# Kernel optimization log

Measured on AMD Instinct MI355X. Metric: run time of the kernel, lower is better.

Reference implementation:

```python
import jax, jax.numpy as jnp
import numpy as np

HIDDEN = 1024
N_HEADS = 16
HEAD_DIM = HIDDEN // N_HEADS
SCALE = HEAD_DIM ** (-0.5)


def setup_inputs() -> dict:
    key = jax.random.key(0)
    k1, k2, k3 = jax.random.split(key, 3)
    x = jax.random.normal(k1, (2, 2048, HIDDEN), dtype=jnp.float32)
    w_qkv = jax.random.normal(k2, (HIDDEN, 3 * HIDDEN), dtype=jnp.float32) * (HIDDEN ** -0.5)
    b_qkv = jnp.zeros((3 * HIDDEN,), dtype=jnp.float32)
    w_proj = jax.random.normal(k3, (HIDDEN, HIDDEN), dtype=jnp.float32) * (HIDDEN ** -0.5)
    b_proj = jnp.zeros((HIDDEN,), dtype=jnp.float32)
    return {"x": x, "w_qkv": w_qkv, "b_qkv": b_qkv, "w_proj": w_proj, "b_proj": b_proj}


def reference(x, w_qkv, b_qkv, w_proj, b_proj):
    b, n, dim = x.shape
    qkv = x @ w_qkv + b_qkv                              # (b, n, 3*dim)
    qkv = qkv.reshape(b, n, 3, N_HEADS, HEAD_DIM)
    qkv = jnp.transpose(qkv, (2, 0, 3, 1, 4))            # (3, b, h, n, d)
    q, k, v = qkv[0], qkv[1], qkv[2]
    dp = jnp.einsum('bhqd,bhkd->bhqk', q, k) * SCALE     # (b, h, n, n)
    # NOTE: original applies softmax over dim=1 == the HEADS axis (non-standard)
    attn = jax.nn.softmax(dp, axis=1)
    w_avg = jnp.einsum('bhqk,bhkd->bhqd', attn, v)       # (b, h, n, d)
    w_avg = jnp.transpose(w_avg, (0, 2, 1, 3)).reshape(b, n, dim)
    out = w_avg @ w_proj + b_proj
    return out
```

## Files before the change

### kernel.cpp

```cpp
#include <hip/hip_runtime.h>

typedef unsigned short u16;
typedef unsigned int u32;
typedef __attribute__((ext_vector_type(8))) short bf16x8;
typedef __attribute__((ext_vector_type(4))) float f32x4;
typedef __attribute__((ext_vector_type(8))) u16 u16x8;

__device__ __forceinline__ u16 f2b(float f){
  u32 u = __float_as_uint(f);
  u32 r = (u + 0x7fffu + ((u >> 16) & 1u)) >> 16;
  return (u16)r;
}
__device__ __forceinline__ float b2f(u16 h){ return __uint_as_float(((u32)h) << 16); }
__device__ __forceinline__ u32 cvt_pk_bf16(float lo, float hi){
  u32 r; asm("v_cvt_pk_bf16_f32 %0, %1, %2" : "=v"(r) : "v"(lo), "v"(hi)); return r;
}

typedef const __attribute__((address_space(1))) void gvoid;
typedef __attribute__((address_space(3))) void svoid;
__device__ __forceinline__ void gl_lds16(const void* g, void* l){
  __builtin_amdgcn_global_load_lds((gvoid*)g, (svoid*)l, 16, 0, 0);
}

__global__ void conv_f2b(const float* __restrict__ in, u16* __restrict__ out, int n8){
  int i = blockIdx.x * 256 + threadIdx.x;
  if(i >= n8) return;
  f32x4 a = *(const f32x4*)(in + (size_t)i*8);
  f32x4 b = *(const f32x4*)(in + (size_t)i*8 + 4);
  u16x8 o;
  #pragma unroll
  for(int j=0;j<4;j++){ o[j] = f2b(a[j]); o[4+j] = f2b(b[j]); }
  *(u16x8*)(out + (size_t)i*8) = o;
}

__global__ void tconv(const float* __restrict__ in, u16* __restrict__ out, int R, int C){
  __shared__ __align__(16) float tile[64*68];
  int gc = C >> 6;
  int rt = blockIdx.x / gc, ct = blockIdx.x % gc;
  int r0 = rt*64, c0 = ct*64;
  int tid = threadIdx.x;
  #pragma unroll
  for(int it=0; it<4; it++){
    int idx = tid + it*256;
    int rl = idx >> 4, cseg = idx & 15;
    f32x4 v = *(const f32x4*)(in + (size_t)(r0+rl)*C + c0 + cseg*4);
    *(f32x4*)&tile[rl*68 + cseg*4] = v;
  }
  __syncthreads();
  #pragma unroll
  for(int it=0; it<2; it++){
    int idx = tid + it*256;
    int cl = idx >> 3, rseg = idx & 7;
    u16x8 o;
    #pragma unroll
    for(int j=0;j<8;j++) o[j] = f2b(tile[(rseg*8+j)*68 + cl]);
    *(u16x8*)(out + (size_t)(c0+cl)*R + r0 + rseg*8) = o;
  }
}

template<int EPI>
__global__ __launch_bounds__(256,2) void gemm_bt(const u16* __restrict__ A, const u16* __restrict__ Bt,
                                                 void* __restrict__ Cp, const float* __restrict__ bias,
                                                 int M, int N, int K){
  __shared__ __align__(16) u16 As[128*32];
  __shared__ __align__(16) u16 Bs[128*32];
  int tid = threadIdx.x, lane = tid & 63, w = tid >> 6;
  int nb = N >> 7;
  int bm = blockIdx.x / nb, bn = blockIdx.x % nb;
  int m0 = bm*128, n0 = bn*128;
  int wm = (w >> 1)*64, wn = (w & 1)*64;
  int l16 = lane & 15, lg = lane >> 4;
  f32x4 acc[4][4];
  #pragma unroll
  for(int i=0;i<4;i++)
    #pragma unroll
    for(int j=0;j<4;j++) acc[i][j] = (f32x4){0.f,0.f,0.f,0.f};

  for(int kk=0; kk<K; kk+=32){
    #pragma unroll
    for(int it=0; it<2; it++){
      int id = tid + it*256;
      int row = id >> 2, seg = id & 3;
      gl_lds16(A  + (size_t)(m0+row)*K + kk + seg*8, &As[id*8]);
      gl_lds16(Bt + (size_t)(n0+row)*K + kk + seg*8, &Bs[id*8]);
    }
    __syncthreads();
    bf16x8 af[4], bfr[4];
    #pragma unroll
    for(int i=0;i<4;i++) af[i]  = *(const bf16x8*)&As[(wm + i*16 + l16)*32 + lg*8];
    #pragma unroll
    for(int j=0;j<4;j++) bfr[j] = *(const bf16x8*)&Bs[(wn + j*16 + l16)*32 + lg*8];
    #pragma unroll
    for(int i=0;i<4;i++)
      #pragma unroll
      for(int j=0;j<4;j++)
        acc[i][j] = __builtin_amdgcn_mfma_f32_16x16x32_bf16(af[i], bfr[j], acc[i][j], 0,0,0);
    __syncthreads();
  }
  #pragma unroll
  for(int i=0;i<4;i++)
    #pragma unroll
    for(int j=0;j<4;j++){
      int col = n0 + wn + j*16 + l16;
      #pragma unroll
      for(int r=0;r<4;r++){
        int row = m0 + wm + i*16 + lg*4 + r;
        float v = acc[i][j][r];
        if(EPI == 0) ((u16*)Cp)[(size_t)row*N + col] = f2b(v);
        else         ((float*)Cp)[(size_t)row*N + col] = v + bias[col];
      }
    }
}

__global__ void scatter_qk(const u16* __restrict__ qkv, const float* __restrict__ bqkv,
                           u16* __restrict__ Qs, u16* __restrict__ Ks){
  int v = blockIdx.x * 256 + threadIdx.x;
  int which = v >> 19;
  int idx8 = v & 524287;
  int o = idx8 << 3;
  int b = o >> 21, h = (o >> 17) & 15, n = (o >> 6) & 2047, d0 = o & 63;
  const u16* src = qkv + (size_t)(b*2048 + n)*3072 + which*1024 + h*64 + d0;
  u16x8 raw = *(const u16x8*)src;
  const float* bp = bqkv + which*1024 + h*64 + d0;
  f32x4 b0 = *(const f32x4*)bp, b1 = *(const f32x4*)(bp + 4);
  float scale = (which == 0) ? 0.18033688011112042f : 1.0f;
  u16x8 ov;
  #pragma unroll
  for(int j=0;j<4;j++){
    ov[j]   = f2b((b2f(raw[j])   + b0[j]) * scale);
    ov[4+j] = f2b((b2f(raw[4+j]) + b1[j]) * scale);
  }
  u16* dst = (which ? Ks : Qs) + o;
  *(u16x8*)dst = ov;
}

__global__ void transpose_v(const u16* __restrict__ qkv, u16* __restrict__ Vt){
  __shared__ __align__(16) u16 tile[64*72];
  int nt = blockIdx.x & 31, bh = blockIdx.x >> 5;
  int b = bh >> 4, h = bh & 15;
  int n0 = nt*64;
  int tid = threadIdx.x;
  const u16* src = qkv + (size_t)(b*2048)*3072 + 2048 + h*64;
  #pragma unroll
  for(int it=0; it<2; it++){
    int idx = tid + it*256;
    int nl = idx >> 3, dseg = idx & 7;
    u16x8 vv = *(const u16x8*)(src + (size_t)(n0+nl)*3072 + dseg*8);
    *(u16x8*)&tile[nl*72 + dseg*8] = vv;
  }
  __syncthreads();
  u16* dst = Vt + (size_t)bh*64*2048;
  #pragma unroll
  for(int it=0; it<2; it++){
    int idx = tid + it*256;
    int dl = idx >> 3, nseg = idx & 7;
    u16x8 o;
    #pragma unroll
    for(int j=0;j<8;j++) o[j] = tile[(nseg*8+j)*72 + dl];
    *(u16x8*)(dst + (size_t)dl*2048 + n0 + nseg*8) = o;
  }
}

#define PROW 40
__global__ __launch_bounds__(512,2) void attn_kernel(const u16* __restrict__ Q, const u16* __restrict__ Kg,
                                                     const u16* __restrict__ Vt, u16* __restrict__ Op){
  __shared__ __align__(16) u16 Pall[16*32*PROW];
  __shared__ __align__(16) float rZs[32*36];
  const int tid = threadIdx.x, lane = tid & 63, w = tid >> 6;
  const int l16 = lane & 15, lg = lane >> 4;
  const int bid = blockIdx.x;
  const int split = bid & 1, qt = (bid >> 1) & 63, b = bid >> 7;
  const int q0 = qt*32;
  const int kbase = split*1024;

  const u16* Kh[2]; const u16* Vh[2];
  #pragma unroll
  for(int hh=0;hh<2;hh++){
    int h = w*2 + hh;
    Kh[hh] = Kg + (size_t)(b*16 + h)*2048*64;
    Vh[hh] = Vt + (size_t)(b*16 + h)*64*2048;
  }

  bf16x8 qf[2][2][2];
  #pragma unroll
  for(int hh=0;hh<2;hh++){
    int h = w*2 + hh;
    const u16* Qh = Q + ((size_t)(b*16 + h)*2048 + q0)*64;
    #pragma unroll
    for(int qs=0;qs<2;qs++)
      #pragma unroll
      for(int dc=0;dc<2;dc++)
        qf[hh][qs][dc] = *(const bf16x8*)(Qh + (qs*16 + l16)*64 + dc*32 + lg*8);
  }
  f32x4 Oa[2][2][4];
  #pragma unroll
  for(int a=0;a<2;a++)
    #pragma unroll
    for(int c=0;c<2;c++)
      #pragma unroll
      for(int d=0;d<4;d++) Oa[a][c][d] = (f32x4){0.f,0.f,0.f,0.f};

  bf16x8 kfb[2][2][2][2];
  #pragma unroll
  for(int hh=0;hh<2;hh++)
    #pragma unroll
    for(int ks=0;ks<2;ks++)
      #pragma unroll
      for(int dc=0;dc<2;dc++)
        kfb[0][hh][ks][dc] = *(const bf16x8*)(Kh[hh] + (size_t)(kbase + ks*16 + l16)*64 + dc*32 + lg*8);

  #pragma unroll 2
  for(int kt=0; kt<32; kt++){
    const int cur = kt & 1, nxt = cur ^ 1;
    const int k0 = kbase + kt*32;
    const int k1 = (kt == 31) ? kbase : k0 + 32;

    bf16x8 vf[2][4];
    #pragma unroll
    for(int hh=0;hh<2;hh++)
      #pragma unroll
      for(int ds=0;ds<4;ds++)
        vf[hh][ds] = *(const bf16x8*)(Vh[hh] + (size_t)(ds*16 + l16)*2048 + k0 + lg*8);

    #pragma unroll
    for(int hh=0;hh<2;hh++){
      int h = w*2 + hh;
      f32x4 S[2][2];
      #pragma unroll
      for(int qs=0;qs<2;qs++)
        #pragma unroll
        for(int ks=0;ks<2;ks++) S[qs][ks] = (f32x4){0.f,0.f,0.f,0.f};
      #pragma unroll
      for(int ks=0;ks<2;ks++)
        #pragma unroll
        for(int dc=0;dc<2;dc++){
          #pragma unroll
          for(int qs=0;qs<2;qs++)
            S[qs][ks] = __builtin_amdgcn_mfma_f32_16x16x32_bf16(qf[hh][qs][dc], kfb[cur][hh][ks][dc], S[qs][ks], 0,0,0);
        }
      u16* Ph = &Pall[(h*32)*PROW];
      #pragma unroll
      for(int qs=0;qs<2;qs++)
        #pragma unroll
        for(int ks=0;ks<2;ks++){
          int q = qs*16 + lg*4;
          int k = ks*16 + l16;
          float e0 = __builtin_amdgcn_exp2f(S[qs][ks][0]);
          float e1 = __builtin_amdgcn_exp2f(S[qs][ks][1]);
          float e2 = __builtin_amdgcn_exp2f(S[qs][ks][2]);
          float e3 = __builtin_amdgcn_exp2f(S[qs][ks][3]);
          u32 w01 = cvt_pk_bf16(e0, e1);
          u32 w23 = cvt_pk_bf16(e2, e3);
          Ph[(q + 0)*PROW + k] = (u16)w01;
          Ph[(q + 1)*PROW + k] = (u16)(w01 >> 16);
          Ph[(q + 2)*PROW + k] = (u16)w23;
          Ph[(q + 3)*PROW + k] = (u16)(w23 >> 16);
        }
    }

    #pragma unroll
    for(int hh=0;hh<2;hh++)
      #pragma unroll
      for(int ks=0;ks<2;ks++)
        #pragma unroll
        for(int dc=0;dc<2;dc++)
          kfb[nxt][hh][ks][dc] = *(const bf16x8*)(Kh[hh] + (size_t)(k1 + ks*16 + l16)*64 + dc*32 + lg*8);

    __syncthreads();
    #pragma unroll
    for(int rr=0; rr<2; rr++){
      int ee = tid + rr*512;
      int q = ee >> 5, k = ee & 31;
      float z = 0.f;
      #pragma unroll
      for(int h=0; h<16; h++) z += b2f(Pall[(h*32 + q)*PROW + k]);
      rZs[q*36 + k] = __builtin_amdgcn_rcpf(z);
    }
    __syncthreads();
    #pragma unroll
    for(int hh=0;hh<2;hh++){
      int h = w*2 + hh;
      bf16x8 pf[2];
      #pragma unroll
      for(int qs=0;qs<2;qs++){
        int q = qs*16 + l16;
        u16x8 praw = *(const u16x8*)&Pall[(h*32 + q)*PROW + lg*8];
        const float* rzp = &rZs[q*36 + lg*8];
        f32x4 rz0 = *(const f32x4*)rzp;
        f32x4 rz1 = *(const f32x4*)(rzp + 4);
        union { u32 wd[4]; bf16x8 v; } U;
        U.wd[0] = cvt_pk_bf16(b2f(praw[0])*rz0[0], b2f(praw[1])*rz0[1]);
        U.wd[1] = cvt_pk_bf16(b2f(praw[2])*rz0[2], b2f(praw[3])*rz0[3]);
        U.wd[2] = cvt_pk_bf16(b2f(praw[4])*rz1[0], b2f(praw[5])*rz1[1]);
        U.wd[3] = cvt_pk_bf16(b2f(praw[6])*rz1[2], b2f(praw[7])*rz1[3]);
        pf[qs] = U.v;
      }
      #pragma unroll
      for(int ds=0;ds<4;ds++){
        #pragma unroll
        for(int qs=0;qs<2;qs++)
          Oa[hh][qs][ds] = __builtin_amdgcn_mfma_f32_16x16x32_bf16(pf[qs], vf[hh][ds], Oa[hh][qs][ds], 0,0,0);
      }
    }
    __syncthreads();
  }
  u16* Ob = Op + (size_t)split*4194304;
  #pragma unroll
  for(int hh=0;hh<2;hh++){
    int h = w*2 + hh;
    #pragma unroll
    for(int qs=0;qs<2;qs++)
      #pragma unroll
      for(int ds=0;ds<4;ds++){
        int col = h*64 + ds*16 + l16;
        #pragma unroll
        for(int r=0;r<4;r++){
          int row = q0 + qs*16 + lg*4 + r;
          Ob[(size_t)(b*2048 + row)*1024 + col] = f2b(Oa[hh][qs][ds][r]);
        }
      }
  }
}

__global__ void combine2(const u16* __restrict__ a, const u16* __restrict__ b, u16* __restrict__ o){
  int i = blockIdx.x * 256 + threadIdx.x;
  u16x8 va = ((const u16x8*)a)[i], vb = ((const u16x8*)b)[i];
  u16x8 vo;
  #pragma unroll
  for(int j=0;j<8;j++) vo[j] = f2b(b2f(va[j]) + b2f(vb[j]));
  ((u16x8*)o)[i] = vo;
}

extern "C" void kernel_launch(void* const* d_in, const int* in_sizes, int n_in,
                              void* d_out, int out_size, void* d_ws, size_t ws_size,
                              hipStream_t stream){
  const float* x      = (const float*)d_in[0];
  const float* w_qkv  = (const float*)d_in[1];
  const float* b_qkv  = (const float*)d_in[2];
  const float* w_proj = (const float*)d_in[3];
  const float* b_proj = (const float*)d_in[4];
  float* out = (float*)d_out;
  char* ws = (char*)d_ws;

  u16* xb   = (u16*)(ws);
  u16* wqT  = (u16*)(ws + 8388608);
  u16* wpT  = (u16*)(ws + 14680064);
  u16* Qs   = (u16*)(ws + 16777216);
  u16* Ks   = (u16*)(ws + 25165824);
  u16* Vt   = (u16*)(ws + 33554432);
  u16* qkvb = (u16*)(ws + 41943040);
  u16* Op0  = qkvb;
  u16* Op1  = qkvb + 4194304;
  u16* wavg = xb;

  conv_f2b<<<2048, 256, 0, stream>>>(x, xb, 524288);
  tconv<<<768, 256, 0, stream>>>(w_qkv, wqT, 1024, 3072);
  tconv<<<256, 256, 0, stream>>>(w_proj, wpT, 1024, 1024);
  gemm_bt<0><<<768, 256, 0, stream>>>(xb, wqT, (void*)qkvb, nullptr, 4096, 3072, 1024);
  scatter_qk<<<4096, 256, 0, stream>>>(qkvb, b_qkv, Qs, Ks);
  transpose_v<<<1024, 256, 0, stream>>>(qkvb, Vt);
  attn_kernel<<<256, 512, 0, stream>>>(Qs, Ks, Vt, Op0);
  combine2<<<2048, 256, 0, stream>>>(Op0, Op1, wavg);
  gemm_bt<1><<<256, 256, 0, stream>>>(wavg, wpT, (void*)out, b_proj, 4096, 1024, 1024);
}
```

Before: 224.7 us.

## Keep softmax probabilities in registers and exchange via ds_bpermute instead of LDS

The attention kernel now computes transposed score tiles (K as the A operand) so each lane holds its exp values in registers. Only per-wave partial head sums (in fp32) go to LDS for the cross-head denominator, and the normalized P fragments are rearranged into MFMA operand layout with ds_bpermute rather than being written to and re-read from a bf16 LDS buffer. The PV product is also transposed, so output stores become packed 8-byte writes, and the trailing block barrier is dropped. This cuts LDS traffic and one sync per iteration, at the cost of more bpermute instructions, more live registers, and reliance on the zsum/rz reuse being safe without a final barrier.

```diff
diff --git a/kernel.cpp b/kernel.cpp
--- a/kernel.cpp
+++ b/kernel.cpp
@@ -5,6 +5,7 @@
 typedef __attribute__((ext_vector_type(8))) short bf16x8;
 typedef __attribute__((ext_vector_type(4))) float f32x4;
 typedef __attribute__((ext_vector_type(8))) u16 u16x8;
+typedef __attribute__((ext_vector_type(2))) u32 u32x2;
 
 __device__ __forceinline__ u16 f2b(float f){
   u32 u = __float_as_uint(f);
@@ -14,6 +15,11 @@
 __device__ __forceinline__ float b2f(u16 h){ return __uint_as_float(((u32)h) << 16); }
 __device__ __forceinline__ u32 cvt_pk_bf16(float lo, float hi){
   u32 r; asm("v_cvt_pk_bf16_f32 %0, %1, %2" : "=v"(r) : "v"(lo), "v"(hi)); return r;
+}
+__device__ __forceinline__ void lds_barrier(){
+  asm volatile("s_waitcnt lgkmcnt(0)" ::: "memory");
+  __builtin_amdgcn_s_barrier();
+  asm volatile("" ::: "memory");
 }
 
 typedef const __attribute__((address_space(1))) void gvoid;
@@ -161,11 +167,10 @@
   }
 }
 
-#define PROW 40
 __global__ __launch_bounds__(512,2) void attn_kernel(const u16* __restrict__ Q, const u16* __restrict__ Kg,
                                                      const u16* __restrict__ Vt, u16* __restrict__ Op){
-  __shared__ __align__(16) u16 Pall[16*32*PROW];
-  __shared__ __align__(16) float rZs[32*36];
+  __shared__ float zsum[8*1024];
+  __shared__ float rz[1024];
   const int tid = threadIdx.x, lane = tid & 63, w = tid >> 6;
   const int l16 = lane & 15, lg = lane >> 4;
   const int bid = blockIdx.x;
@@ -192,13 +197,13 @@
       for(int dc=0;dc<2;dc++)
         qf[hh][qs][dc] = *(const bf16x8*)(Qh + (qs*16 + l16)*64 + dc*32 + lg*8);
   }
-  f32x4 Oa[2][2][4];
+  f32x4 Oa[2][4][2];
   #pragma unroll
   for(int a=0;a<2;a++)
     #pragma unroll
-    for(int c=0;c<2;c++)
-      #pragma unroll
-      for(int d=0;d<4;d++) Oa[a][c][d] = (f32x4){0.f,0.f,0.f,0.f};
+    for(int d=0;d<4;d++)
+      #pragma unroll
+      for(int c=0;c<2;c++) Oa[a][d][c] = (f32x4){0.f,0.f,0.f,0.f};
 
   bf16x8 kfb[2][2][2][2];
   #pragma unroll
@@ -208,6 +213,9 @@
       #pragma unroll
       for(int dc=0;dc<2;dc++)
         kfb[0][hh][ks][dc] = *(const bf16x8*)(Kh[hh] + (size_t)(kbase + ks*16 + l16)*64 + dc*32 + lg*8);
+
+  const int bp0 = ((2*(lg & 1))*16 + l16)*4;
+  const int bp1 = bp0 + 64;
 
   #pragma unroll 2
   for(int kt=0; kt<32; kt++){
@@ -219,44 +227,31 @@
     #pragma unroll
     for(int hh=0;hh<2;hh++)
       #pragma unroll
-      for(int ds=0;ds<4;ds++)
-        vf[hh][ds] = *(const bf16x8*)(Vh[hh] + (size_t)(ds*16 + l16)*2048 + k0 + lg*8);
-
-    #pragma unroll
-    for(int hh=0;hh<2;hh++){
-      int h = w*2 + hh;
-      f32x4 S[2][2];
+      for(int dt=0;dt<4;dt++)
+        vf[hh][dt] = *(const bf16x8*)(Vh[hh] + (size_t)(dt*16 + l16)*2048 + k0 + lg*8);
+
+    float p[2][2][2][4];
+    #pragma unroll
+    for(int hh=0;hh<2;hh++)
       #pragma unroll
       for(int qs=0;qs<2;qs++)
         #pragma unroll
-        for(int ks=0;ks<2;ks++) S[qs][ks] = (f32x4){0.f,0.f,0.f,0.f};
+        for(int ks=0;ks<2;ks++){
+          f32x4 S = (f32x4){0.f,0.f,0.f,0.f};
+          #pragma unroll
+          for(int dc=0;dc<2;dc++)
+            S = __builtin_amdgcn_mfma_f32_16x16x32_bf16(kfb[cur][hh][ks][dc], qf[hh][qs][dc], S, 0,0,0);
+          #pragma unroll
+          for(int r=0;r<4;r++) p[hh][qs][ks][r] = __builtin_amdgcn_exp2f(S[r]);
+        }
+
+    #pragma unroll
+    for(int qs=0;qs<2;qs++)
       #pragma unroll
       for(int ks=0;ks<2;ks++)
         #pragma unroll
-        for(int dc=0;dc<2;dc++){
-          #pragma unroll
-          for(int qs=0;qs<2;qs++)
-            S[qs][ks] = __builtin_amdgcn_mfma_f32_16x16x32_bf16(qf[hh][qs][dc], kfb[cur][hh][ks][dc], S[qs][ks], 0,0,0);
-        }
-      u16* Ph = &Pall[(h*32)*PROW];
-      #pragma unroll
-      for(int qs=0;qs<2;qs++)
-        #pragma unroll
-        for(int ks=0;ks<2;ks++){
-          int q = qs*16 + lg*4;
-          int k = ks*16 + l16;
-          float e0 = __builtin_amdgcn_exp2f(S[qs][ks][0]);
-          float e1 = __builtin_amdgcn_exp2f(S[qs][ks][1]);
-          float e2 = __builtin_amdgcn_exp2f(S[qs][ks][2]);
-          float e3 = __builtin_amdgcn_exp2f(S[qs][ks][3]);
-          u32 w01 = cvt_pk_bf16(e0, e1);
-          u32 w23 = cvt_pk_bf16(e2, e3);
-          Ph[(q + 0)*PROW + k] = (u16)w01;
-          Ph[(q + 1)*PROW + k] = (u16)(w01 >> 16);
-          Ph[(q + 2)*PROW + k] = (u16)w23;
-          Ph[(q + 3)*PROW + k] = (u16)(w23 >> 16);
-        }
-    }
+        for(int r=0;r<4;r++)
+          zsum[w*1024 + (qs*2+ks)*256 + r*64 + lane] = p[0][qs][ks][r] + p[1][qs][ks][r];
 
     #pragma unroll
     for(int hh=0;hh<2;hh++)
@@ -266,58 +261,65 @@
         for(int dc=0;dc<2;dc++)
           kfb[nxt][hh][ks][dc] = *(const bf16x8*)(Kh[hh] + (size_t)(k1 + ks*16 + l16)*64 + dc*32 + lg*8);
 
-    __syncthreads();
+    lds_barrier();
     #pragma unroll
     for(int rr=0; rr<2; rr++){
-      int ee = tid + rr*512;
-      int q = ee >> 5, k = ee & 31;
+      int s = tid + rr*512;
       float z = 0.f;
       #pragma unroll
-      for(int h=0; h<16; h++) z += b2f(Pall[(h*32 + q)*PROW + k]);
-      rZs[q*36 + k] = __builtin_amdgcn_rcpf(z);
+      for(int wv=0; wv<8; wv++) z += zsum[wv*1024 + s];
+      rz[s] = __builtin_amdgcn_rcpf(z);
     }
-    __syncthreads();
+    lds_barrier();
+
     #pragma unroll
     for(int hh=0;hh<2;hh++){
-      int h = w*2 + hh;
-      bf16x8 pf[2];
       #pragma unroll
       for(int qs=0;qs<2;qs++){
-        int q = qs*16 + l16;
-        u16x8 praw = *(const u16x8*)&Pall[(h*32 + q)*PROW + lg*8];
-        const float* rzp = &rZs[q*36 + lg*8];
-        f32x4 rz0 = *(const f32x4*)rzp;
-        f32x4 rz1 = *(const f32x4*)(rzp + 4);
+        u32 Wa[2], Wb[2];
+        #pragma unroll
+        for(int ks=0;ks<2;ks++){
+          float pn[4];
+          #pragma unroll
+          for(int r=0;r<4;r++)
+            pn[r] = p[hh][qs][ks][r] * rz[(qs*2+ks)*256 + r*64 + lane];
+          Wa[ks] = cvt_pk_bf16(pn[0], pn[1]);
+          Wb[ks] = cvt_pk_bf16(pn[2], pn[3]);
+        }
+        bool lo = (lg < 2);
+        u32 t0a = __builtin_amdgcn_ds_bpermute(bp0, (int)Wa[0]);
+        u32 t0b = __builtin_amdgcn_ds_bpermute(bp0, (int)Wa[1]);
+        u32 t1a = __builtin_amdgcn_ds_bpermute(bp0, (int)Wb[0]);
+        u32 t1b = __builtin_amdgcn_ds_bpermute(bp0, (int)Wb[1]);
+        u32 t2a = __builtin_amdgcn_ds_bpermute(bp1, (int)Wa[0]);
+        u32 t2b = __builtin_amdgcn_ds_bpermute(bp1, (int)Wa[1]);
+        u32 t3a = __builtin_amdgcn_ds_bpermute(bp1, (int)Wb[0]);
+        u32 t3b = __builtin_amdgcn_ds_bpermute(bp1, (int)Wb[1]);
         union { u32 wd[4]; bf16x8 v; } U;
-        U.wd[0] = cvt_pk_bf16(b2f(praw[0])*rz0[0], b2f(praw[1])*rz0[1]);
-        U.wd[1] = cvt_pk_bf16(b2f(praw[2])*rz0[2], b2f(praw[3])*rz0[3]);
-        U.wd[2] = cvt_pk_bf16(b2f(praw[4])*rz1[0], b2f(praw[5])*rz1[1]);
-        U.wd[3] = cvt_pk_bf16(b2f(praw[6])*rz1[2], b2f(praw[7])*rz1[3]);
-        pf[qs] = U.v;
-      }
-      #pragma unroll
-      for(int ds=0;ds<4;ds++){
-        #pragma unroll
-        for(int qs=0;qs<2;qs++)
-          Oa[hh][qs][ds] = __builtin_amdgcn_mfma_f32_16x16x32_bf16(pf[qs], vf[hh][ds], Oa[hh][qs][ds], 0,0,0);
+        U.wd[0] = lo ? t0a : t0b;
+        U.wd[1] = lo ? t1a : t1b;
+        U.wd[2] = lo ? t2a : t2b;
+        U.wd[3] = lo ? t3a : t3b;
+        #pragma unroll
+        for(int dt=0;dt<4;dt++)
+          Oa[hh][dt][qs] = __builtin_amdgcn_mfma_f32_16x16x32_bf16(vf[hh][dt], U.v, Oa[hh][dt][qs], 0,0,0);
       }
     }
-    __syncthreads();
   }
   u16* Ob = Op + (size_t)split*4194304;
   #pragma unroll
   for(int hh=0;hh<2;hh++){
     int h = w*2 + hh;
     #pragma unroll
-    for(int qs=0;qs<2;qs++)
-      #pragma unroll
-      for(int ds=0;ds<4;ds++){
-        int col = h*64 + ds*16 + l16;
-        #pragma unroll
-        for(int r=0;r<4;r++){
-          int row = q0 + qs*16 + lg*4 + r;
-          Ob[(size_t)(b*2048 + row)*1024 + col] = f2b(Oa[hh][qs][ds][r]);
-        }
+    for(int dt=0;dt<4;dt++)
+      #pragma unroll
+      for(int qs=0;qs<2;qs++){
+        int row = q0 + qs*16 + l16;
+        int col = h*64 + dt*16 + lg*4;
+        u32x2 pk2;
+        pk2[0] = cvt_pk_bf16(Oa[hh][dt][qs][0], Oa[hh][dt][qs][1]);
+        pk2[1] = cvt_pk_bf16(Oa[hh][dt][qs][2], Oa[hh][dt][qs][3]);
+        *(u32x2*)(Ob + (size_t)(b*2048 + row)*1024 + col) = pk2;
       }
   }
 }
```

Result: faster. 220.3 us (-2.0%).
